# Kernel tuning notes

Measured on AMD Instinct MI355X. Metric: run time of the kernel, lower is better.

## Reference

```python
import jax, jax.numpy as jnp
import numpy as np

N_NODES = 20000
N_EDGES = 320000
F_DIM = 64      # num_features == hidden_units
HID = 64
N_RUNS = 10
N_GRAPHS = 128
N_CLASSES = 10
N_LAYERS = 4
BN_EPS = 1e-5
P_DROP = 0.2


def _batchnorm(t, g, b):
    # training-mode BatchNorm1d over the flattened (num_runs*N, d) rows, biased variance
    mu = jnp.mean(t, axis=0)
    var = jnp.mean(jnp.square(t - mu), axis=0)
    return (t - mu) * jax.lax.rsqrt(var + BN_EPS) * g + b


def setup_inputs() -> dict:
    key = jax.random.key(0)
    ks = jax.random.split(key, 16)
    x = jax.random.normal(ks[0], (N_NODES, F_DIM), jnp.float32)
    edge_index = jax.random.randint(ks[1], (2, N_EDGES), 0, N_NODES, dtype=jnp.int32)
    batch = jnp.sort(jax.random.randint(ks[2], (N_NODES,), 0, N_GRAPHS, dtype=jnp.int32))
    drop_mask = jax.random.uniform(ks[3], (N_RUNS, N_NODES)) < P_DROP
    s = 0.1
    conv_w1 = jax.random.normal(ks[4], (N_LAYERS, F_DIM, HID), jnp.float32) * s
    conv_b1 = jax.random.normal(ks[5], (N_LAYERS, HID), jnp.float32) * s
    bn1_g = jax.random.uniform(ks[6], (N_LAYERS, HID), jnp.float32, 0.5, 1.5)
    bn1_b = jax.random.normal(ks[7], (N_LAYERS, HID), jnp.float32) * s
    conv_w2 = jax.random.normal(ks[8], (N_LAYERS, HID, HID), jnp.float32) * s
    conv_b2 = jax.random.normal(ks[9], (N_LAYERS, HID), jnp.float32) * s
    bn_g = jax.random.uniform(ks[10], (N_LAYERS, HID), jnp.float32, 0.5, 1.5)
    bn_b = jax.random.normal(ks[11], (N_LAYERS, HID), jnp.float32) * s
    fc_w = jax.random.normal(ks[12], (N_LAYERS + 1, HID, N_CLASSES), jnp.float32) * s
    fc_b = jax.random.normal(ks[13], (N_LAYERS + 1, N_CLASSES), jnp.float32) * s
    return dict(x=x, edge_index=edge_index, batch=batch, drop_mask=drop_mask,
                conv_w1=conv_w1, conv_b1=conv_b1, bn1_g=bn1_g, bn1_b=bn1_b,
                conv_w2=conv_w2, conv_b2=conv_b2, bn_g=bn_g, bn_b=bn_b,
                fc_w=fc_w, fc_b=fc_b)


def reference(x, edge_index, batch, drop_mask,
              conv_w1, conv_b1, bn1_g, bn1_b, conv_w2, conv_b2, bn_g, bn_b,
              fc_w, fc_b):
    # prediction path (eval): node-drop, 4 GIN layers over num_runs replicated
    # graphs, per-level mean-over-runs + global_add_pool + fc, sum, log_softmax.
    R = drop_mask.shape[0]
    N = x.shape[0]
    src, dst = edge_index[0], edge_index[1]
    # replicated node features with stochastic node drop: [R, N, F]
    h = jnp.where(drop_mask[..., None], jnp.zeros((), x.dtype), x[None])
    outs = [h]
    for i in range(N_LAYERS):
        # GINConv (eps=0): MLP(x + sum_{j->i} x_j); vectorized over runs
        # (equivalent to the original offset-replicated run_edge_index).
        agg = jnp.zeros_like(h).at[:, dst].add(h[:, src])  # [R, N, d]
        z = (h + agg).reshape(R * N, -1)
        t = z @ conv_w1[i] + conv_b1[i]
        t = jax.nn.relu(_batchnorm(t, bn1_g[i], bn1_b[i]))
        t = t @ conv_w2[i] + conv_b2[i]
        t = jax.nn.relu(_batchnorm(t, bn_g[i], bn_b[i]))
        h = t.reshape(R, N, -1)
        outs.append(h)
    out = jnp.zeros((N_GRAPHS, N_CLASSES), x.dtype)
    for i, o in enumerate(outs):
        m = jnp.mean(o, axis=0)  # [N, d] mean over runs
        pooled = jax.ops.segment_sum(m, batch, num_segments=N_GRAPHS)  # global_add_pool
        out = out + pooled @ fc_w[i] + fc_b[i]  # dropout is identity in eval
    return jax.nn.log_softmax(out, axis=-1)
```

## Files before the change

kernel.cpp:

```cpp
#include <hip/hip_runtime.h>

#define N_NODES 20000
#define N_EDGES 320000
#define R_RUNS 10
#define HID 64
#define NG 128
#define NC 10
#define NL 4
#define MROWS (R_RUNS * N_NODES)
#define BN_EPS 1e-5f
#define NCOPY 16
#define TS 72
#define AG_NPB 8
#define G2_TILES 5
#define PB_NPB 16
#define PB_SLOTS 4
#define P0_NPB 32
#define P0_SLOTS 6

typedef __bf16 bf16;
typedef __attribute__((ext_vector_type(8))) __bf16 bf16x8;
typedef __attribute__((ext_vector_type(4))) float f32x4;
typedef unsigned int uint32;

constexpr size_t OFF_FLAGS   = 0;
constexpr size_t OFF_CURSOR  = 256;
constexpr size_t OFF_STATS   = 80640;
constexpr size_t OFF_POOLED5 = 146176;
constexpr size_t ZERO_BYTES  = 310016;
constexpr size_t OFF_ROWST   = 310016;
constexpr size_t OFF_COL     = 390400;
constexpr size_t OFF_PARAMS  = 1670400;
constexpr size_t OFF_XB      = 1745664;
constexpr size_t OFF_H       = 4305664;
constexpr size_t OFF_Z       = 29905664;

#define PW1  0
#define PB1  16384
#define PG1  16640
#define PBB1 16896
#define PW2  17152
#define PB2  33536
#define PG2  33792
#define PBB2 34048
#define PFW  34304
#define PFB  37504
#define PTOT 37554
#define CVT_TOT (1280000 + PTOT)

__global__ void detect_kernel(const unsigned short* __restrict__ xu,
                              const unsigned int* __restrict__ mw,
                              int* __restrict__ cnts) {
    int tid = blockIdx.x * 256 + threadIdx.x;
    int insane = 0, lowp = 0, f32w = 0, gt1 = 0;
    for (int i = tid; i < 4096; i += 16384) {
        unsigned int u = xu[2 * i];
        if (((u >> 7) & 0xFFu) >= 0x90u) insane++;
    }
    for (int i = tid; i < 50000; i += 16384) {
        unsigned int w = mw[i];
        if ((w & 0xFFFFu) == 0x3F80u) lowp = 1;
        else if (w == 0x3F800000u) f32w = 1;
        else if (w > 1u) gt1 = 1;
    }
    if (insane) atomicAdd(&cnts[0], insane);
    if (lowp)   atomicOr(&cnts[1], 1);
    if (f32w)   atomicOr(&cnts[2], 1);
    if (gt1)    atomicOr(&cnts[3], 1);
}

__device__ inline bf16 ld_any(const void* p, int i, int f32mode) {
    if (f32mode) return (bf16)((const float*)p)[i];
    return ((const bf16*)p)[i];
}

__device__ inline int mask_dropped(const void* maskp, const int* cnts, size_t idx) {
    int w = cnts[1] ? 2 : (cnts[2] ? 4 : (cnts[3] ? 1 : 4));
    if (w == 1) return ((const unsigned char*)maskp)[idx] != 0;
    if (w == 2) return ((const unsigned short*)maskp)[idx] != 0;
    return ((const unsigned int*)maskp)[idx] != 0;
}

__global__ void convert_kernel(const int* __restrict__ cnts,
                               const void* x, const void* w1, const void* b1,
                               const void* g1, const void* bb1, const void* w2,
                               const void* b2, const void* g2, const void* bb2,
                               const void* fw, const void* fb,
                               bf16* __restrict__ xb, bf16* __restrict__ params) {
    int t = blockIdx.x * 256 + threadIdx.x;
    if (t >= CVT_TOT) return;
    int f = cnts[0] > 64;
    if (t < 1280000) { xb[t] = ld_any(x, t, f); return; }
    int u = t - 1280000;
    if (u < PB1 || (u >= PW2 && u < PB2)) {
        const void* src = (u < PB1) ? w1 : w2;
        int v = (u < PB1) ? u : u - PW2;
        int layer = v >> 12, rem = v & 4095;
        int j = rem & 7, lane = (rem >> 3) & 63, ntc = rem >> 9;
        int nt = ntc >> 1, c = ntc & 1;
        int k = c * 32 + (lane >> 4) * 8 + j;
        int n = nt * 16 + (lane & 15);
        params[u] = ld_any(src, layer * 4096 + k * 64 + n, f);
        return;
    }
    const void* src; int base;
    if      (u < PG1)  { src = b1;  base = PB1; }
    else if (u < PBB1) { src = g1;  base = PG1; }
    else if (u < PW2)  { src = bb1; base = PBB1; }
    else if (u < PG2)  { src = b2;  base = PB2; }
    else if (u < PBB2) { src = g2;  base = PG2; }
    else if (u < PFW)  { src = bb2; base = PBB2; }
    else if (u < PFB)  { src = fw;  base = PFW; }
    else               { src = fb;  base = PFB; }
    params[u] = ld_any(src, u - base, f);
}

__global__ void build_h0_kernel(const bf16* __restrict__ xb, const void* __restrict__ maskp,
                                const int* __restrict__ cnts, bf16* __restrict__ h) {
    int i = blockIdx.x * 256 + threadIdx.x;
    int c = i & 7;
    int rowid = i >> 3;
    int r = rowid % R_RUNS;
    int n = rowid / R_RUNS;
    int dropped = mask_dropped(maskp, cnts, (size_t)r * N_NODES + n);
    bf16x8 v;
    if (dropped) {
        #pragma unroll
        for (int j = 0; j < 8; ++j) v[j] = (bf16)0.0f;
    } else {
        v = *(const bf16x8*)(xb + (size_t)n * HID + c * 8);
    }
    *(bf16x8*)(h + (size_t)rowid * HID + c * 8) = v;
}

__global__ __launch_bounds__(256) void pool0_kernel(const bf16* __restrict__ xb,
                                                    const void* __restrict__ maskp,
                                                    const int* __restrict__ cnts,
                                                    const int* __restrict__ batch,
                                                    float* __restrict__ pooled) {
    __shared__ float lp[P0_SLOTS][64];
    __shared__ float lcnt[P0_NPB];
    __shared__ int gfirst;
    int tid = threadIdx.x;
    for (int i = tid; i < P0_SLOTS * 64; i += 256) ((float*)lp)[i] = 0.f;
    if (tid == 0) gfirst = batch[blockIdx.x * P0_NPB];
    if (tid < P0_NPB) {
        int n = blockIdx.x * P0_NPB + tid;
        int cnt = 0;
        #pragma unroll
        for (int r = 0; r < R_RUNS; ++r)
            cnt += !mask_dropped(maskp, cnts, (size_t)r * N_NODES + n);
        lcnt[tid] = (float)cnt * (1.0f / R_RUNS);
    }
    __syncthreads();
    int c = tid & 7, ln = tid >> 3;
    int n = blockIdx.x * P0_NPB + ln;
    bf16x8 xv = *(const bf16x8*)(xb + (size_t)n * HID + c * 8);
    float sc = lcnt[ln];
    int g = batch[n];
    int slot = g - gfirst;
    if (slot < P0_SLOTS) {
        #pragma unroll
        for (int j = 0; j < 8; ++j)
            atomicAdd(&lp[slot][c * 8 + j], (float)xv[j] * sc);
    } else {
        #pragma unroll
        for (int j = 0; j < 8; ++j)
            atomicAdd(&pooled[g * HID + c * 8 + j], (float)xv[j] * sc);
    }
    __syncthreads();
    for (int s = tid >> 6; s < P0_SLOTS; s += 4) {
        int f = tid & 63;
        float v = lp[s][f];
        if (v != 0.f) atomicAdd(&pooled[(gfirst + s) * HID + f], v);
    }
}

__global__ void csr_count_kernel(const int* __restrict__ ei, int* __restrict__ deg) {
    int e = blockIdx.x * 256 + threadIdx.x;
    if (e < N_EDGES) atomicAdd(&deg[ei[N_EDGES + e]], 1);
}

__global__ void csr_scan_kernel(int* __restrict__ deg, int* __restrict__ row_start) {
    __shared__ int lds[1024];
    int tid = threadIdx.x;
    const int CH = 20;
    int base = tid * CH;
    int local[CH];
    int s = 0;
    #pragma unroll
    for (int j = 0; j < CH; ++j) {
        int n = base + j;
        int d = (n < N_NODES) ? deg[n] : 0;
        local[j] = d; s += d;
    }
    lds[tid] = s; __syncthreads();
    for (int off = 1; off < 1024; off <<= 1) {
        int add = (tid >= off) ? lds[tid - off] : 0;
        __syncthreads();
        lds[tid] += add;
        __syncthreads();
    }
    int excl = lds[tid] - s;
    #pragma unroll
    for (int j = 0; j < CH; ++j) {
        int n = base + j;
        if (n < N_NODES) { row_start[n] = excl; deg[n] = excl; excl += local[j]; }
    }
    if (tid == 1023) row_start[N_NODES] = lds[1023];
}

__global__ void csr_fill_kernel(const int* __restrict__ ei, int* __restrict__ cursor,
                                int* __restrict__ col) {
    int e = blockIdx.x * 256 + threadIdx.x;
    if (e < N_EDGES) {
        int src = ei[e];
        int dst = ei[N_EDGES + e];
        int pos = atomicAdd(&cursor[dst], 1);
        col[pos] = src;
    }
}

__global__ __launch_bounds__(256) void ag1_kernel(const uint32* __restrict__ hD,
                                                  const int* __restrict__ row_start,
                                                  const int* __restrict__ col,
                                                  const bf16* __restrict__ Wf,
                                                  const bf16* __restrict__ bias,
                                                  bf16* __restrict__ out,
                                                  float* __restrict__ statsOut) {
    __shared__ __align__(16) bf16 zT[AG_NPB * R_RUNS * TS];
    __shared__ float lsum[64], lsq[64];
    uint32* zTu = (uint32*)zT;
    int tid = threadIdx.x;
    int wave = tid >> 6, lane = tid & 63, l16 = lane & 15, quad = lane >> 4;
    int b = blockIdx.x;
    const int NODE_DW = R_RUNS * HID / 2;

    if (tid < 64) { lsum[tid] = 0.f; lsq[tid] = 0.f; }

    for (int i = 0; i < AG_NPB / 4; ++i) {
        int nl = wave + 4 * i;
        int n = b * AG_NPB + nl;
        size_t base4 = (size_t)n * NODE_DW + lane * 4;
        size_t baset = (size_t)n * NODE_DW + 256 + lane;
        float acc[10];
        {
            uint4 u = *(const uint4*)(hD + base4);
            uint32 tw = hD[baset];
            acc[0] = __uint_as_float(u.x << 16); acc[1] = __uint_as_float(u.x & 0xFFFF0000u);
            acc[2] = __uint_as_float(u.y << 16); acc[3] = __uint_as_float(u.y & 0xFFFF0000u);
            acc[4] = __uint_as_float(u.z << 16); acc[5] = __uint_as_float(u.z & 0xFFFF0000u);
            acc[6] = __uint_as_float(u.w << 16); acc[7] = __uint_as_float(u.w & 0xFFFF0000u);
            acc[8] = __uint_as_float(tw << 16);  acc[9] = __uint_as_float(tw & 0xFFFF0000u);
        }
        int beg = row_start[n], end = row_start[n + 1];
        int idx = beg;
        for (; idx + 4 <= end; idx += 4) {
            uint4 a[4]; uint32 tw[4];
            #pragma unroll
            for (int u = 0; u < 4; ++u) {
                size_t o = (size_t)col[idx + u] * NODE_DW;
                a[u] = *(const uint4*)(hD + o + lane * 4);
                tw[u] = hD[o + 256 + lane];
            }
            #pragma unroll
            for (int u = 0; u < 4; ++u) {
                uint32 wd[4] = {a[u].x, a[u].y, a[u].z, a[u].w};
                #pragma unroll
                for (int c = 0; c < 4; ++c) {
                    acc[2 * c]     += __uint_as_float(wd[c] << 16);
                    acc[2 * c + 1] += __uint_as_float(wd[c] & 0xFFFF0000u);
                }
                acc[8] += __uint_as_float(tw[u] << 16);
                acc[9] += __uint_as_float(tw[u] & 0xFFFF0000u);
            }
        }
        for (; idx < end; ++idx) {
            size_t o = (size_t)col[idx] * NODE_DW;
            uint4 a0 = *(const uint4*)(hD + o + lane * 4);
            uint32 t0 = hD[o + 256 + lane];
            uint32 wd[4] = {a0.x, a0.y, a0.z, a0.w};
            #pragma unroll
            for (int c = 0; c < 4; ++c) {
                acc[2 * c]     += __uint_as_float(wd[c] << 16);
                acc[2 * c + 1] += __uint_as_float(wd[c] & 0xFFFF0000u);
            }
            acc[8] += __uint_as_float(t0 << 16);
            acc[9] += __uint_as_float(t0 & 0xFFFF0000u);
        }
        #pragma unroll
        for (int c = 0; c < 5; ++c) {
            int d = (c < 4) ? (lane * 4 + c) : (256 + lane);
            int rL = nl * R_RUNS + (d >> 5);
            int fp = d & 31;
            unsigned short lo = __builtin_bit_cast(unsigned short, (bf16)acc[2 * c]);
            unsigned short hi = __builtin_bit_cast(unsigned short, (bf16)acc[2 * c + 1]);
            zTu[rL * (TS / 2) + fp] = (uint32)lo | ((uint32)hi << 16);
        }
    }
    __syncthreads();

    bf16x8 bfr[4][2];
    #pragma unroll
    for (int nt = 0; nt < 4; ++nt)
        #pragma unroll
        for (int c = 0; c < 2; ++c)
            bfr[nt][c] = *(const bf16x8*)(Wf + (size_t)((nt * 2 + c) * 64 + lane) * 8);
    float bvs[4];
    #pragma unroll
    for (int nt = 0; nt < 4; ++nt) bvs[nt] = (float)bias[nt * 16 + l16];

    for (int g = wave; g < 5; g += 4) {
        const bf16* tp = &zT[(g * 16 + l16) * TS];
        bf16x8 a0 = *(const bf16x8*)(tp + quad * 8);
        bf16x8 a1 = *(const bf16x8*)(tp + 32 + quad * 8);
        f32x4 acc[4];
        #pragma unroll
        for (int nt = 0; nt < 4; ++nt) acc[nt] = (f32x4){bvs[nt], bvs[nt], bvs[nt], bvs[nt]};
        #pragma unroll
        for (int nt = 0; nt < 4; ++nt) {
            acc[nt] = __builtin_amdgcn_mfma_f32_16x16x32_bf16(a0, bfr[nt][0], acc[nt], 0, 0, 0);
            acc[nt] = __builtin_amdgcn_mfma_f32_16x16x32_bf16(a1, bfr[nt][1], acc[nt], 0, 0, 0);
        }
        size_t rowBase = (size_t)b * (AG_NPB * R_RUNS) + g * 16;
        #pragma unroll
        for (int nt = 0; nt < 4; ++nt) {
            float ss = 0.f, qq = 0.f;
            #pragma unroll
            for (int reg = 0; reg < 4; ++reg) {
                float v = acc[nt][reg];
                ss += v; qq += v * v;
                out[(rowBase + quad * 4 + reg) * HID + nt * 16 + l16] = (bf16)v;
            }
            atomicAdd(&lsum[nt * 16 + l16], ss);
            atomicAdd(&lsq[nt * 16 + l16], qq);
        }
    }
    __syncthreads();
    if (tid < 64) {
        int copy = b & (NCOPY - 1);
        atomicAdd(&statsOut[copy * 128 + tid], lsum[tid]);
        atomicAdd(&statsOut[copy * 128 + 64 + tid], lsq[tid]);
    }
}

__global__ __launch_bounds__(256) void gemm64_kernel(const bf16* in,
                                                     const bf16* __restrict__ Wf,
                                                     const bf16* __restrict__ bias,
                                                     bf16* out,
                                                     const float* __restrict__ statsIn,
                                                     const bf16* __restrict__ gammaIn,
                                                     const bf16* __restrict__ betaIn,
                                                     float* __restrict__ statsOut) {
    __shared__ float lstat[128];
    __shared__ float lscale[64], lshift[64];
    __shared__ float lsum[64], lsq[64];
    int tid = threadIdx.x;
    int wave = tid >> 6, lane = tid & 63, l16 = lane & 15, quad = lane >> 4;

    if (tid < 128) {
        float s = 0.f;
        #pragma unroll
        for (int k = 0; k < NCOPY; ++k) s += statsIn[k * 128 + tid];
        lstat[tid] = s;
    }
    if (tid < 64) { lsum[tid] = 0.f; lsq[tid] = 0.f; }
    __syncthreads();
    if (tid < 64) {
        float mu = lstat[tid] * (1.0f / MROWS);
        float var = lstat[tid + 64] * (1.0f / MROWS) - mu * mu;
        float rs = rsqrtf(var + BN_EPS);
        float a = (float)gammaIn[tid] * rs;
        lscale[tid] = a;
        lshift[tid] = (float)betaIn[tid] - mu * a;
    }
    __syncthreads();

    bf16x8 bfrag[4][2];
    #pragma unroll
    for (int nt = 0; nt < 4; ++nt)
        #pragma unroll
        for (int c = 0; c < 2; ++c)
            bfrag[nt][c] = *(const bf16x8*)(Wf + (size_t)((nt * 2 + c) * 64 + lane) * 8);
    float bvs[4];
    #pragma unroll
    for (int nt = 0; nt < 4; ++nt) bvs[nt] = (float)bias[nt * 16 + l16];

    for (int t5 = 0; t5 < G2_TILES; ++t5) {
        size_t rowBase = (size_t)blockIdx.x * (G2_TILES * 64) + t5 * 64 + wave * 16;
        f32x4 acc[4];
        #pragma unroll
        for (int nt = 0; nt < 4; ++nt) acc[nt] = (f32x4){bvs[nt], bvs[nt], bvs[nt], bvs[nt]};

        size_t row = rowBase + l16;
        bf16x8 afrag[2];
        #pragma unroll
        for (int c = 0; c < 2; ++c) {
            int k0 = c * 32 + quad * 8;
            bf16x8 v = *(const bf16x8*)(in + row * HID + k0);
            #pragma unroll
            for (int j = 0; j < 8; ++j) {
                float f = (float)v[j] * lscale[k0 + j] + lshift[k0 + j];
                v[j] = (bf16)fmaxf(f, 0.f);
            }
            afrag[c] = v;
        }

        #pragma unroll
        for (int nt = 0; nt < 4; ++nt) {
            acc[nt] = __builtin_amdgcn_mfma_f32_16x16x32_bf16(afrag[0], bfrag[nt][0], acc[nt], 0, 0, 0);
            acc[nt] = __builtin_amdgcn_mfma_f32_16x16x32_bf16(afrag[1], bfrag[nt][1], acc[nt], 0, 0, 0);
        }

        #pragma unroll
        for (int nt = 0; nt < 4; ++nt) {
            float s = 0.f, q = 0.f;
            #pragma unroll
            for (int reg = 0; reg < 4; ++reg) {
                float v = acc[nt][reg];
                s += v; q += v * v;
                out[(rowBase + quad * 4 + reg) * HID + nt * 16 + l16] = (bf16)v;
            }
            atomicAdd(&lsum[nt * 16 + l16], s);
            atomicAdd(&lsq[nt * 16 + l16], q);
        }
    }
    __syncthreads();
    if (tid < 64) {
        int copy = blockIdx.x & (NCOPY - 1);
        atomicAdd(&statsOut[copy * 128 + tid], lsum[tid]);
        atomicAdd(&statsOut[copy * 128 + 64 + tid], lsq[tid]);
    }
}

__global__ __launch_bounds__(256) void pool_bn_kernel(const bf16* __restrict__ t,
                                                      const float* __restrict__ statsIn,
                                                      const bf16* __restrict__ gammaIn,
                                                      const bf16* __restrict__ betaIn,
                                                      bf16* __restrict__ hOut,
                                                      const int* __restrict__ batch,
                                                      float* __restrict__ pooled) {
    __shared__ float lstat[128], lscale[64], lshift[64];
    __shared__ float lp[PB_SLOTS][64];
    __shared__ int gfirst;
    int tid = threadIdx.x;
    if (tid < 128) {
        float s = 0.f;
        #pragma unroll
        for (int k = 0; k < NCOPY; ++k) s += statsIn[k * 128 + tid];
        lstat[tid] = s;
    }
    for (int i = tid; i < PB_SLOTS * 64; i += 256) ((float*)lp)[i] = 0.f;
    if (tid == 0) gfirst = batch[blockIdx.x * PB_NPB];
    __syncthreads();
    if (tid < 64) {
        float mu = lstat[tid] * (1.0f / MROWS);
        float var = lstat[tid + 64] * (1.0f / MROWS) - mu * mu;
        float rs = rsqrtf(var + BN_EPS);
        float a = (float)gammaIn[tid] * rs;
        lscale[tid] = a;
        lshift[tid] = (float)betaIn[tid] - mu * a;
    }
    __syncthreads();
    int f = tid & 63, nsub = tid >> 6;
    float sc = lscale[f], sh = lshift[f];
    #pragma unroll
    for (int j = 0; j < PB_NPB / 4; ++j) {
        int n = blockIdx.x * PB_NPB + j * 4 + nsub;
        size_t base = (size_t)n * (R_RUNS * HID) + f;
        float s = 0.f;
        #pragma unroll
        for (int r = 0; r < R_RUNS; ++r) {
            float v = (float)t[base + r * HID];
            v = fmaxf(v * sc + sh, 0.f);
            hOut[base + r * HID] = (bf16)v;
            s += v;
        }
        int g = batch[n];
        int slot = g - gfirst;
        if (slot < PB_SLOTS) atomicAdd(&lp[slot][f], s * (1.0f / R_RUNS));
        else                 atomicAdd(&pooled[g * HID + f], s * (1.0f / R_RUNS));
    }
    __syncthreads();
    for (int s = tid >> 6; s < PB_SLOTS; s += 4) {
        float v = lp[s][tid & 63];
        if (v != 0.f) atomicAdd(&pooled[(gfirst + s) * HID + (tid & 63)], v);
    }
}

__global__ void fc_softmax_kernel(const float* __restrict__ pooled5,
                                  const bf16* __restrict__ params,
                                  const int* __restrict__ cnts, void* __restrict__ out) {
    int g = threadIdx.x;
    if (g >= NG) return;
    float o[NC];
    #pragma unroll
    for (int c = 0; c < NC; ++c) o[c] = 0.f;
    for (int l = 0; l < NL + 1; ++l) {
        const float* pg = pooled5 + ((size_t)l * NG + g) * HID;
        const bf16* fw = params + PFW + l * (HID * NC);
        for (int k = 0; k < HID; ++k) {
            float p = pg[k];
            #pragma unroll
            for (int c = 0; c < NC; ++c) o[c] += p * (float)fw[k * NC + c];
        }
        #pragma unroll
        for (int c = 0; c < NC; ++c) o[c] += (float)params[PFB + l * NC + c];
    }
    float m = -1e30f;
    #pragma unroll
    for (int c = 0; c < NC; ++c) m = fmaxf(m, o[c]);
    float s = 0.f;
    #pragma unroll
    for (int c = 0; c < NC; ++c) s += expf(o[c] - m);
    float lg = logf(s);
    int f = cnts[0] > 64;
    #pragma unroll
    for (int c = 0; c < NC; ++c) {
        float val = o[c] - m - lg;
        if (f) ((float*)out)[g * NC + c] = val;
        else   ((bf16*)out)[g * NC + c] = (bf16)val;
    }
}

extern "C" void kernel_launch(void* const* d_in, const int* in_sizes, int n_in,
                              void* d_out, int out_size, void* d_ws, size_t ws_size,
                              hipStream_t stream) {
    const void* x     = d_in[0];
    const int*  ei    = (const int*)d_in[1];
    const int*  batch = (const int*)d_in[2];
    const void* maskp = d_in[3];

    char* ws = (char*)d_ws;
    int*   cnts    = (int*)(ws + OFF_FLAGS);
    int*   cursor  = (int*)(ws + OFF_CURSOR);
    float* statsb  = (float*)(ws + OFF_STATS);
    float* pooled5 = (float*)(ws + OFF_POOLED5);
    int*   rowst   = (int*)(ws + OFF_ROWST);
    int*   colbuf  = (int*)(ws + OFF_COL);
    bf16*  params  = (bf16*)(ws + OFF_PARAMS);
    bf16*  xb      = (bf16*)(ws + OFF_XB);
    bf16*  h       = (bf16*)(ws + OFF_H);
    bf16*  z       = (bf16*)(ws + OFF_Z);

    hipMemsetAsync(ws, 0, ZERO_BYTES, stream);

    detect_kernel<<<64, 256, 0, stream>>>((const unsigned short*)x,
                                          (const unsigned int*)maskp, cnts);
    convert_kernel<<<(CVT_TOT + 255) / 256, 256, 0, stream>>>(
        cnts, x, d_in[4], d_in[5], d_in[6], d_in[7], d_in[8], d_in[9], d_in[10],
        d_in[11], d_in[12], d_in[13], xb, params);

    csr_count_kernel<<<(N_EDGES + 255) / 256, 256, 0, stream>>>(ei, cursor);
    csr_scan_kernel<<<1, 1024, 0, stream>>>(cursor, rowst);
    csr_fill_kernel<<<(N_EDGES + 255) / 256, 256, 0, stream>>>(ei, cursor, colbuf);

    build_h0_kernel<<<(MROWS * 8) / 256, 256, 0, stream>>>(xb, maskp, cnts, h);
    pool0_kernel<<<N_NODES / P0_NPB, 256, 0, stream>>>(xb, maskp, cnts, batch, pooled5);

    for (int i = 0; i < NL; ++i) {
        float* st1 = statsb + (size_t)(2 * i) * (NCOPY * 128);
        float* st2 = statsb + (size_t)(2 * i + 1) * (NCOPY * 128);

        ag1_kernel<<<N_NODES / AG_NPB, 256, 0, stream>>>(
            (const uint32*)h, rowst, colbuf,
            params + PW1 + i * 4096, params + PB1 + i * 64, z, st1);

        gemm64_kernel<<<MROWS / (G2_TILES * 64), 256, 0, stream>>>(
            z, params + PW2 + i * 4096, params + PB2 + i * 64, z,
            st1, params + PG1 + i * 64, params + PBB1 + i * 64, st2);

        pool_bn_kernel<<<N_NODES / PB_NPB, 256, 0, stream>>>(
            z, st2, params + PG2 + i * 64, params + PBB2 + i * 64, h, batch,
            pooled5 + (size_t)(i + 1) * NG * HID);
    }

    fc_softmax_kernel<<<1, 128, 0, stream>>>(pooled5, params, cnts, d_out);
}
```

Before: 772.8 us.

## Specialize first GIN layer aggregation to read base features with per-node drop bitmask

The layer-0 aggregation no longer materializes the replicated [R,N,64] drop-masked feature tensor. A new kernel gathers the single shared bf16 feature row per neighbor and applies a 10-bit per-node drop mask (written by pool0) to accumulate all runs at once. This removes the build_h0 kernel and cuts the layer-0 gather traffic roughly by the run count. The cost is more per-lane conditional adds and a cross-half shuffle reduction.

```diff
diff --git a/kernel.cpp b/kernel.cpp
--- a/kernel.cpp
+++ b/kernel.cpp
@@ -23,6 +23,9 @@
 typedef __attribute__((ext_vector_type(4))) float f32x4;
 typedef unsigned int uint32;
 
+__device__ inline float blo(uint32 u) { return __uint_as_float(u << 16); }
+__device__ inline float bhi(uint32 u) { return __uint_as_float(u & 0xFFFF0000u); }
+
 constexpr size_t OFF_FLAGS   = 0;
 constexpr size_t OFF_CURSOR  = 256;
 constexpr size_t OFF_STATS   = 80640;
@@ -30,10 +33,11 @@
 constexpr size_t ZERO_BYTES  = 310016;
 constexpr size_t OFF_ROWST   = 310016;
 constexpr size_t OFF_COL     = 390400;
-constexpr size_t OFF_PARAMS  = 1670400;
-constexpr size_t OFF_XB      = 1745664;
-constexpr size_t OFF_H       = 4305664;
-constexpr size_t OFF_Z       = 29905664;
+constexpr size_t OFF_KB      = 1670400;
+constexpr size_t OFF_PARAMS  = 1750528;
+constexpr size_t OFF_XB      = 1825792;
+constexpr size_t OFF_H       = 4385792;
+constexpr size_t OFF_Z       = 29985792;
 
 #define PW1  0
 #define PB1  16384
@@ -115,29 +119,12 @@
     params[u] = ld_any(src, u - base, f);
 }
 
-__global__ void build_h0_kernel(const bf16* __restrict__ xb, const void* __restrict__ maskp,
-                                const int* __restrict__ cnts, bf16* __restrict__ h) {
-    int i = blockIdx.x * 256 + threadIdx.x;
-    int c = i & 7;
-    int rowid = i >> 3;
-    int r = rowid % R_RUNS;
-    int n = rowid / R_RUNS;
-    int dropped = mask_dropped(maskp, cnts, (size_t)r * N_NODES + n);
-    bf16x8 v;
-    if (dropped) {
-        #pragma unroll
-        for (int j = 0; j < 8; ++j) v[j] = (bf16)0.0f;
-    } else {
-        v = *(const bf16x8*)(xb + (size_t)n * HID + c * 8);
-    }
-    *(bf16x8*)(h + (size_t)rowid * HID + c * 8) = v;
-}
-
 __global__ __launch_bounds__(256) void pool0_kernel(const bf16* __restrict__ xb,
                                                     const void* __restrict__ maskp,
                                                     const int* __restrict__ cnts,
                                                     const int* __restrict__ batch,
-                                                    float* __restrict__ pooled) {
+                                                    float* __restrict__ pooled,
+                                                    int* __restrict__ kb) {
     __shared__ float lp[P0_SLOTS][64];
     __shared__ float lcnt[P0_NPB];
     __shared__ int gfirst;
@@ -146,11 +133,15 @@
     if (tid == 0) gfirst = batch[blockIdx.x * P0_NPB];
     if (tid < P0_NPB) {
         int n = blockIdx.x * P0_NPB + tid;
-        int cnt = 0;
-        #pragma unroll
-        for (int r = 0; r < R_RUNS; ++r)
-            cnt += !mask_dropped(maskp, cnts, (size_t)r * N_NODES + n);
+        int cnt = 0, kbv = 0;
+        #pragma unroll
+        for (int r = 0; r < R_RUNS; ++r) {
+            int d = mask_dropped(maskp, cnts, (size_t)r * N_NODES + n);
+            kbv |= d << r;
+            cnt += !d;
+        }
         lcnt[tid] = (float)cnt * (1.0f / R_RUNS);
+        kb[n] = kbv;
     }
     __syncthreads();
     int c = tid & 7, ln = tid >> 3;
@@ -218,6 +209,130 @@
         int dst = ei[N_EDGES + e];
         int pos = atomicAdd(&cursor[dst], 1);
         col[pos] = src;
+    }
+}
+
+__global__ __launch_bounds__(256) void ag1_l1_kernel(const uint32* __restrict__ xbD,
+                                                     const int* __restrict__ kb,
+                                                     const int* __restrict__ row_start,
+                                                     const int* __restrict__ col,
+                                                     const bf16* __restrict__ Wf,
+                                                     const bf16* __restrict__ bias,
+                                                     bf16* __restrict__ out,
+                                                     float* __restrict__ statsOut) {
+    __shared__ __align__(16) bf16 zT[AG_NPB * R_RUNS * TS];
+    __shared__ float lsum[64], lsq[64];
+    uint32* zTu = (uint32*)zT;
+    int tid = threadIdx.x;
+    int wave = tid >> 6, lane = tid & 63, l16 = lane & 15, quad = lane >> 4;
+    int p = lane & 31, hf = lane >> 5;
+    int b = blockIdx.x;
+
+    if (tid < 64) { lsum[tid] = 0.f; lsq[tid] = 0.f; }
+
+    for (int i = 0; i < AG_NPB / 4; ++i) {
+        int nl = wave + 4 * i;
+        int n = b * AG_NPB + nl;
+        float ax[R_RUNS], ay[R_RUNS];
+        {
+            uint32 xs = xbD[(size_t)n * 32 + p];
+            int ms = kb[n];
+            float fx = blo(xs), fy = bhi(xs);
+            #pragma unroll
+            for (int r = 0; r < R_RUNS; ++r) {
+                int keep = (hf == 0) && !((ms >> r) & 1);
+                ax[r] = keep ? fx : 0.f;
+                ay[r] = keep ? fy : 0.f;
+            }
+        }
+        int beg = row_start[n], end = row_start[n + 1];
+        int iters = (end - beg + 1) >> 1;
+        int k = 0;
+        for (; k + 4 <= iters; k += 4) {
+            uint32 xv[4]; int mv[4];
+            #pragma unroll
+            for (int u = 0; u < 4; ++u) {
+                int idx = beg + 2 * (k + u) + hf;
+                int valid = idx < end;
+                int j = valid ? col[idx] : n;
+                xv[u] = xbD[(size_t)j * 32 + p];
+                mv[u] = valid ? kb[j] : 0x3FF;
+            }
+            #pragma unroll
+            for (int u = 0; u < 4; ++u) {
+                float fx = blo(xv[u]), fy = bhi(xv[u]);
+                #pragma unroll
+                for (int r = 0; r < R_RUNS; ++r)
+                    if (!((mv[u] >> r) & 1)) { ax[r] += fx; ay[r] += fy; }
+            }
+        }
+        for (; k < iters; ++k) {
+            int idx = beg + 2 * k + hf;
+            int valid = idx < end;
+            int j = valid ? col[idx] : n;
+            uint32 xv = xbD[(size_t)j * 32 + p];
+            int mv = valid ? kb[j] : 0x3FF;
+            float fx = blo(xv), fy = bhi(xv);
+            #pragma unroll
+            for (int r = 0; r < R_RUNS; ++r)
+                if (!((mv >> r) & 1)) { ax[r] += fx; ay[r] += fy; }
+        }
+        #pragma unroll
+        for (int r = 0; r < R_RUNS; ++r) {
+            ax[r] += __shfl_xor(ax[r], 32);
+            ay[r] += __shfl_xor(ay[r], 32);
+        }
+        #pragma unroll
+        for (int q = 0; q < 5; ++q) {
+            int r = hf * 5 + q;
+            unsigned short lo = __builtin_bit_cast(unsigned short, (bf16)ax[r]);
+            unsigned short hi = __builtin_bit_cast(unsigned short, (bf16)ay[r]);
+            zTu[(nl * R_RUNS + r) * (TS / 2) + p] = (uint32)lo | ((uint32)hi << 16);
+        }
+    }
+    __syncthreads();
+
+    bf16x8 bfr[4][2];
+    #pragma unroll
+    for (int nt = 0; nt < 4; ++nt)
+        #pragma unroll
+        for (int c = 0; c < 2; ++c)
+            bfr[nt][c] = *(const bf16x8*)(Wf + (size_t)((nt * 2 + c) * 64 + lane) * 8);
+    float bvs[4];
+    #pragma unroll
+    for (int nt = 0; nt < 4; ++nt) bvs[nt] = (float)bias[nt * 16 + l16];
+
+    for (int g = wave; g < 5; g += 4) {
+        const bf16* tp = &zT[(g * 16 + l16) * TS];
+        bf16x8 a0 = *(const bf16x8*)(tp + quad * 8);
+        bf16x8 a1 = *(const bf16x8*)(tp + 32 + quad * 8);
+        f32x4 acc[4];
+        #pragma unroll
+        for (int nt = 0; nt < 4; ++nt) acc[nt] = (f32x4){bvs[nt], bvs[nt], bvs[nt], bvs[nt]};
+        #pragma unroll
+        for (int nt = 0; nt < 4; ++nt) {
+            acc[nt] = __builtin_amdgcn_mfma_f32_16x16x32_bf16(a0, bfr[nt][0], acc[nt], 0, 0, 0);
+            acc[nt] = __builtin_amdgcn_mfma_f32_16x16x32_bf16(a1, bfr[nt][1], acc[nt], 0, 0, 0);
+        }
+        size_t rowBase = (size_t)b * (AG_NPB * R_RUNS) + g * 16;
+        #pragma unroll
+        for (int nt = 0; nt < 4; ++nt) {
+            float ss = 0.f, qq = 0.f;
+            #pragma unroll
+            for (int reg = 0; reg < 4; ++reg) {
+                float v = acc[nt][reg];
+                ss += v; qq += v * v;
+                out[(rowBase + quad * 4 + reg) * HID + nt * 16 + l16] = (bf16)v;
+            }
+            atomicAdd(&lsum[nt * 16 + l16], ss);
+            atomicAdd(&lsq[nt * 16 + l16], qq);
+        }
+    }
+    __syncthreads();
+    if (tid < 64) {
+        int copy = b & (NCOPY - 1);
+        atomicAdd(&statsOut[copy * 128 + tid], lsum[tid]);
+        atomicAdd(&statsOut[copy * 128 + 64 + tid], lsq[tid]);
     }
 }
 
@@ -247,11 +362,11 @@
         {
             uint4 u = *(const uint4*)(hD + base4);
             uint32 tw = hD[baset];
-            acc[0] = __uint_as_float(u.x << 16); acc[1] = __uint_as_float(u.x & 0xFFFF0000u);
-            acc[2] = __uint_as_float(u.y << 16); acc[3] = __uint_as_float(u.y & 0xFFFF0000u);
-            acc[4] = __uint_as_float(u.z << 16); acc[5] = __uint_as_float(u.z & 0xFFFF0000u);
-            acc[6] = __uint_as_float(u.w << 16); acc[7] = __uint_as_float(u.w & 0xFFFF0000u);
-            acc[8] = __uint_as_float(tw << 16);  acc[9] = __uint_as_float(tw & 0xFFFF0000u);
+            acc[0] = blo(u.x); acc[1] = bhi(u.x);
+            acc[2] = blo(u.y); acc[3] = bhi(u.y);
+            acc[4] = blo(u.z); acc[5] = bhi(u.z);
+            acc[6] = blo(u.w); acc[7] = bhi(u.w);
+            acc[8] = blo(tw);  acc[9] = bhi(tw);
         }
         int beg = row_start[n], end = row_start[n + 1];
         int idx = beg;
@@ -268,11 +383,11 @@
                 uint32 wd[4] = {a[u].x, a[u].y, a[u].z, a[u].w};
                 #pragma unroll
                 for (int c = 0; c < 4; ++c) {
-                    acc[2 * c]     += __uint_as_float(wd[c] << 16);
-                    acc[2 * c + 1] += __uint_as_float(wd[c] & 0xFFFF0000u);
+                    acc[2 * c]     += blo(wd[c]);
+                    acc[2 * c + 1] += bhi(wd[c]);
                 }
-                acc[8] += __uint_as_float(tw[u] << 16);
-                acc[9] += __uint_as_float(tw[u] & 0xFFFF0000u);
+                acc[8] += blo(tw[u]);
+                acc[9] += bhi(tw[u]);
             }
         }
         for (; idx < end; ++idx) {
@@ -282,11 +397,11 @@
             uint32 wd[4] = {a0.x, a0.y, a0.z, a0.w};
             #pragma unroll
             for (int c = 0; c < 4; ++c) {
-                acc[2 * c]     += __uint_as_float(wd[c] << 16);
-                acc[2 * c + 1] += __uint_as_float(wd[c] & 0xFFFF0000u);
-            }
-            acc[8] += __uint_as_float(t0 << 16);
-            acc[9] += __uint_as_float(t0 & 0xFFFF0000u);
+                acc[2 * c]     += blo(wd[c]);
+                acc[2 * c + 1] += bhi(wd[c]);
+            }
+            acc[8] += blo(t0);
+            acc[9] += bhi(t0);
         }
         #pragma unroll
         for (int c = 0; c < 5; ++c) {
@@ -538,6 +653,7 @@
     float* pooled5 = (float*)(ws + OFF_POOLED5);
     int*   rowst   = (int*)(ws + OFF_ROWST);
     int*   colbuf  = (int*)(ws + OFF_COL);
+    int*   kbuf    = (int*)(ws + OFF_KB);
     bf16*  params  = (bf16*)(ws + OFF_PARAMS);
     bf16*  xb      = (bf16*)(ws + OFF_XB);
     bf16*  h       = (bf16*)(ws + OFF_H);
@@ -555,16 +671,22 @@
     csr_scan_kernel<<<1, 1024, 0, stream>>>(cursor, rowst);
     csr_fill_kernel<<<(N_EDGES + 255) / 256, 256, 0, stream>>>(ei, cursor, colbuf);
 
-    build_h0_kernel<<<(MROWS * 8) / 256, 256, 0, stream>>>(xb, maskp, cnts, h);
-    pool0_kernel<<<N_NODES / P0_NPB, 256, 0, stream>>>(xb, maskp, cnts, batch, pooled5);
+    pool0_kernel<<<N_NODES / P0_NPB, 256, 0, stream>>>(xb, maskp, cnts, batch,
+                                                       pooled5, kbuf);
 
     for (int i = 0; i < NL; ++i) {
         float* st1 = statsb + (size_t)(2 * i) * (NCOPY * 128);
         float* st2 = statsb + (size_t)(2 * i + 1) * (NCOPY * 128);
 
-        ag1_kernel<<<N_NODES / AG_NPB, 256, 0, stream>>>(
-            (const uint32*)h, rowst, colbuf,
-            params + PW1 + i * 4096, params + PB1 + i * 64, z, st1);
+        if (i == 0) {
+            ag1_l1_kernel<<<N_NODES / AG_NPB, 256, 0, stream>>>(
+                (const uint32*)xb, kbuf, rowst, colbuf,
+                params + PW1, params + PB1, z, st1);
+        } else {
+            ag1_kernel<<<N_NODES / AG_NPB, 256, 0, stream>>>(
+                (const uint32*)h, rowst, colbuf,
+                params + PW1 + i * 4096, params + PB1 + i * 64, z, st1);
+        }
 
         gemm64_kernel<<<MROWS / (G2_TILES * 64), 256, 0, stream>>>(
             z, params + PW2 + i * 4096, params + PB2 + i * 64, z,
```

Result: faster. 734.2 us (-5.0%).
